# Kernel optimization log

Hardware: AMD Instinct MI355X
Metric: run time of the kernel (lower is better)

Reference implementation:

```python
import jax, jax.numpy as jnp
import numpy as np
import math

B, L, D_IN, H, N, NL, D_OUT = 16, 4096, 64, 256, 32, 4, 10
EPS = 1e-5


def setup_inputs() -> dict:
    key = jax.random.key(0)
    ks = jax.random.split(key, 16)
    inp = {}
    inp['x'] = jax.random.normal(ks[0], (B, L, D_IN), dtype=jnp.float32)
    inp['enc_w'] = jax.random.normal(ks[1], (H, D_IN), dtype=jnp.float32) / math.sqrt(D_IN)
    inp['enc_b'] = jax.random.normal(ks[2], (H,), dtype=jnp.float32) * 0.01
    # log_dt uniform in [log(1e-3), log(1e-1)] as in S4D init
    inp['log_dt'] = jax.random.uniform(ks[3], (NL, H), dtype=jnp.float32,
                                       minval=math.log(1e-3), maxval=math.log(1e-1))
    inp['log_A_real'] = jnp.full((NL, H, N), math.log(0.5), dtype=jnp.float32)
    inp['A_imag'] = jnp.broadcast_to(math.pi * jnp.arange(N, dtype=jnp.float32), (NL, H, N)).copy()
    inp['C_re'] = jax.random.normal(ks[4], (NL, H, N), dtype=jnp.float32)
    inp['C_im'] = jax.random.normal(ks[5], (NL, H, N), dtype=jnp.float32)
    inp['D'] = jax.random.normal(ks[6], (NL, H), dtype=jnp.float32)
    inp['out_w'] = jax.random.normal(ks[7], (NL, 2 * H, H), dtype=jnp.float32) / math.sqrt(H)
    inp['out_b'] = jax.random.normal(ks[8], (NL, 2 * H), dtype=jnp.float32) * 0.01
    inp['ln_w'] = jnp.ones((NL, H), dtype=jnp.float32)
    inp['ln_b'] = jnp.zeros((NL, H), dtype=jnp.float32)
    inp['dec_w'] = jax.random.normal(ks[9], (D_OUT, H), dtype=jnp.float32) / math.sqrt(H)
    inp['dec_b'] = jax.random.normal(ks[10], (D_OUT,), dtype=jnp.float32) * 0.01
    return inp


def _s4d_kernel(log_dt, log_A_real, A_imag, C_re, C_im, length):
    # log_dt: (H,), others: (H, N). Returns real conv kernel (H, length).
    dt = jnp.exp(log_dt)[:, None]                       # (H, 1)
    A = -jnp.exp(log_A_real) + 1j * A_imag              # (H, N), Re(A) < 0
    dtA = A * dt                                        # (H, N)
    C = (C_re + 1j * C_im) * (jnp.expm1(dtA)) / A       # ZOH-style scaling
    t = jnp.arange(length, dtype=jnp.float32)
    vand = jnp.exp(dtA[:, :, None] * t)                 # (H, N, L) Vandermonde
    K = 2.0 * jnp.real(jnp.einsum('hn,hnl->hl', C, vand))
    return K


def _fft_conv(u, k):
    # u: (B, H, L), k: (H, L) -> causal circular-padded conv, (B, H, L)
    length = u.shape[-1]
    k_f = jnp.fft.rfft(k, n=2 * length)                 # (H, L+1)
    u_f = jnp.fft.rfft(u, n=2 * length)                 # (B, H, L+1)
    return jnp.fft.irfft(u_f * k_f[None], n=2 * length)[..., :length]


def _layernorm_channels(x, w, b):
    # x: (B, H, L), normalize over channel dim H
    mu = jnp.mean(x, axis=1, keepdims=True)
    var = jnp.var(x, axis=1, keepdims=True)
    return (x - mu) * jax.lax.rsqrt(var + EPS) * w[None, :, None] + b[None, :, None]


def reference(x, enc_w, enc_b, log_dt, log_A_real, A_imag, C_re, C_im, D,
              out_w, out_b, ln_w, ln_b, dec_w, dec_b):
    # encoder: (B, L, d_input) -> (B, L, H), then transpose -> (B, H, L)
    h = jnp.einsum('bli,hi->blh', x, enc_w) + enc_b
    h = jnp.swapaxes(h, -1, -2)                         # (B, H, L)
    length = h.shape[-1]
    for i in range(NL):
        z = h
        K = _s4d_kernel(log_dt[i], log_A_real[i], A_imag[i], C_re[i], C_im[i], length)
        y = _fft_conv(z, K) + z * D[i][None, :, None]   # SSM conv + skip
        y = jax.nn.gelu(y)
        # position-wise 1x1 conv to 2H, then GLU over channel dim
        g = jnp.einsum('bhl,gh->bgl', y, out_w[i]) + out_b[i][None, :, None]
        g1, g2 = jnp.split(g, 2, axis=1)
        y = g1 * jax.nn.sigmoid(g2)
        h = y + h                                       # residual (dropout=0)
        h = _layernorm_channels(h, ln_w[i], ln_b[i])    # post-norm
    h = jnp.swapaxes(h, -1, -2)                         # (B, L, H)
    return jnp.einsum('blh,oh->blo', h, dec_w) + dec_b
```

## Files before the change

kernel.cpp:

```cpp
#include <hip/hip_runtime.h>
#include <hip/hip_fp16.h>

#define B_   16
#define L_   4096
#define DIN  64
#define H_   256
#define N_   32
#define NL_  4
#define DOUT 10
#define CH_  32
#define T_   128

typedef _Float16 half8 __attribute__((ext_vector_type(8)));
typedef float f32x4 __attribute__((ext_vector_type(4)));

__device__ __forceinline__ float gelu_f(float v) {
    float t3  = v * v * v;
    float arg = 0.7978845608028654f * fmaf(0.044715f, t3, v);
    float e   = __expf(2.f * arg);
    float th  = 1.f - 2.f / (e + 1.f);
    return 0.5f * v * (1.f + th);
}

__global__ __launch_bounds__(256) void gen_k(
    const float* __restrict__ log_dt, const float* __restrict__ log_A_real,
    const float* __restrict__ A_imag, const float* __restrict__ C_re, const float* __restrict__ C_im,
    const float* __restrict__ Dp,
    _Float16* __restrict__ Wv, _Float16* __restrict__ Vt, _Float16* __restrict__ G,
    float* __restrict__ wtr, float* __restrict__ wti)
{
    __shared__ float sxr[N_], sxi[N_], scr[N_], sci[N_], skd[T_];
    int ih = blockIdx.x;
    int t  = threadIdx.x;
    if (t < N_) {
        int n = t;
        float dt  = expf(log_dt[ih]);
        float Are = -expf(log_A_real[ih * N_ + n]);
        float Aim = A_imag[ih * N_ + n];
        float xr = dt * Are, xi = dt * Aim;
        float ex = expf(xr), cy = cosf(xi), sy = sinf(xi);
        float sh = sinf(0.5f * xi);
        float em_re = expm1f(xr) * cy - 2.f * sh * sh;
        float em_im = ex * sy;
        float inv = 1.f / (Are * Are + Aim * Aim);
        float qr = (em_re * Are + em_im * Aim) * inv;
        float qi = (em_im * Are - em_re * Aim) * inv;
        float crv = C_re[ih * N_ + n], civ = C_im[ih * N_ + n];
        sxr[n] = xr; sxi[n] = xi;
        scr[n] = 2.f * (crv * qr - civ * qi);
        sci[n] = 2.f * (crv * qi + civ * qr);
        float txr = 128.f * xr, txi = 128.f * xi;
        float exT = expf(txr);
        wtr[ih * N_ + n] = exT * cosf(txi);
        wti[ih * N_ + n] = exT * sinf(txi);
    }
    __syncthreads();
    if (t <= T_) {
        int d = t;
        float fd = (float)d;
        float kd = 0.f;
        for (int n = 0; n < N_; n++) {
            float ar = expf(fd * sxr[n]);
            float ang = fd * sxi[n];
            float wdr = ar * cosf(ang), wdi = ar * sinf(ang);
            if (d < T_) {
                kd = fmaf(scr[n], wdr, kd);
                kd = fmaf(-sci[n], wdi, kd);
                Wv[((size_t)ih * 64 + 2 * n) * T_ + (127 - d)]     = (_Float16)wdr;
                Wv[((size_t)ih * 64 + 2 * n + 1) * T_ + (127 - d)] = (_Float16)wdi;
            }
            if (d >= 1) {
                float vr = scr[n] * wdr - sci[n] * wdi;
                float vi = scr[n] * wdi + sci[n] * wdr;
                Vt[((size_t)ih * T_ + (d - 1)) * 64 + 2 * n]     = (_Float16)vr;
                Vt[((size_t)ih * T_ + (d - 1)) * 64 + 2 * n + 1] = (_Float16)(-vi);
            }
        }
        if (d < T_) skd[d] = kd;
    }
    __syncthreads();
    if (t < T_) {
        float v = skd[127 - t];
        if (t == 127) v += Dp[ih];
        G[(size_t)ih * 256 + t]       = (_Float16)v;
        G[(size_t)ih * 256 + 128 + t] = (_Float16)0.f;
    }
}

__global__ __launch_bounds__(256) void wconv_k(const float* __restrict__ w, _Float16* __restrict__ w16)
{
    int idx = blockIdx.x * 256 + threadIdx.x;
    w16[idx] = (_Float16)w[idx];
}

__global__ __launch_bounds__(256) void encoder_k(
    const float* __restrict__ x, const float* __restrict__ ew,
    const float* __restrict__ eb, _Float16* __restrict__ z16)
{
    __shared__ float xt[64][64];
    int blk = blockIdx.x;
    int b  = blk >> 6;
    int l0 = (blk & 63) << 6;
    int t  = threadIdx.x;
    {
        int r = t >> 2, cp = (t & 3) * 16;
        const float4* src = (const float4*)(x + ((size_t)(b * L_ + l0 + r)) * DIN + cp);
        float4* dst = (float4*)&xt[r][cp];
#pragma unroll
        for (int j = 0; j < 4; j++) dst[j] = src[j];
    }
    float wrg[64];
#pragma unroll
    for (int i = 0; i < 64; i += 4) {
        float4 wv = *(const float4*)(ew + t * 64 + i);
        wrg[i] = wv.x; wrg[i+1] = wv.y; wrg[i+2] = wv.z; wrg[i+3] = wv.w;
    }
    float bias = eb[t];
    __syncthreads();
    _Float16* outz = z16 + ((size_t)(b * H_ + t)) * L_ + l0;
    for (int l = 0; l < 64; l += 4) {
        _Float16 h4[4];
#pragma unroll
        for (int q = 0; q < 4; q++) {
            float a0 = 0.f, a1 = 0.f;
#pragma unroll
            for (int i = 0; i < 64; i += 2) {
                a0 = fmaf(xt[l+q][i],   wrg[i],   a0);
                a1 = fmaf(xt[l+q][i+1], wrg[i+1], a1);
            }
            h4[q] = (_Float16)(a0 + a1 + bias);
        }
        *(uint2*)(outz + l) = *(uint2*)h4;
    }
}

__global__ __launch_bounds__(256) void finals_k(
    const _Float16* __restrict__ z16, const _Float16* __restrict__ Wv,
    const float* __restrict__ wtr, const float* __restrict__ wti,
    _Float16* __restrict__ Sinit)
{
    __shared__ _Float16 zb[CH_][136];
    __shared__ float Fs[CH_][68];
    int h = blockIdx.x, b = blockIdx.y;
    int t = threadIdx.x;
    const uint4* src = (const uint4*)(z16 + ((size_t)(b * H_ + h)) * L_);
#pragma unroll
    for (int j = 0; j < 2; j++) {
        uint4 v = src[t * 2 + j];
        int e0 = (t * 2 + j) * 8;
        *(uint4*)&zb[e0 >> 7][e0 & 127] = v;
    }
    __syncthreads();
    int lane = t & 63, w = t >> 6;
    int l15 = lane & 15, quad = lane >> 4;
    f32x4 acc[2];
    acc[0] = (f32x4){0.f,0.f,0.f,0.f};
    acc[1] = (f32x4){0.f,0.f,0.f,0.f};
    const _Float16* wvb = Wv + ((size_t)h * 64 + w * 16 + l15) * T_;
#pragma unroll
    for (int ks = 0; ks < 4; ks++) {
        int kk = ks * 32 + quad * 8;
        half8 a  = *(const half8*)(wvb + kk);
        half8 b0 = *(const half8*)&zb[l15][kk];
        half8 b1 = *(const half8*)&zb[16 + l15][kk];
        acc[0] = __builtin_amdgcn_mfma_f32_16x16x32_f16(a, b0, acc[0], 0, 0, 0);
        acc[1] = __builtin_amdgcn_mfma_f32_16x16x32_f16(a, b1, acc[1], 0, 0, 0);
    }
#pragma unroll
    for (int nt = 0; nt < 2; nt++) {
        int c = nt * 16 + l15;
        *(f32x4*)&Fs[c][w * 16 + quad * 4] = acc[nt];
    }
    __syncthreads();
    if (t < N_) {
        int n = t;
        float wr = wtr[h * N_ + n], wi = wti[h * N_ + n];
        float cr = 0.f, ci = 0.f;
        _Float16* sb = Sinit + ((size_t)(b * H_ + h)) * (CH_ * 64) + 2 * n;
        for (int c = 0; c < CH_; c++) {
            float2 f2 = *(const float2*)&Fs[c][2 * n];
            union { unsigned u; _Float16 hf[2]; } p;
            p.hf[0] = (_Float16)cr; p.hf[1] = (_Float16)ci;
            *(unsigned*)(sb + (size_t)c * 64) = p.u;
            float nr = fmaf(wr, cr, f2.x);
            nr = fmaf(-wi, ci, nr);
            float ni = fmaf(wi, cr, f2.y);
            ni = fmaf(wr, ci, ni);
            cr = nr; ci = ni;
        }
    }
}

__global__ __launch_bounds__(256) void conv_k(
    const _Float16* __restrict__ z16, const _Float16* __restrict__ G,
    const _Float16* __restrict__ Vt, const _Float16* __restrict__ Sinit,
    _Float16* __restrict__ y16)
{
    __shared__ _Float16 zT[128][136];
    __shared__ _Float16 Ff[128][72];
    __shared__ _Float16 Gs[256];
    int h = blockIdx.x, rb = blockIdx.y;
    int t = threadIdx.x;
    int b0 = rb * 4;
#pragma unroll
    for (int q = 0; q < 8; q++) {
        int idx = q * 256 + t;
        int brow = idx >> 9;
        int e = (idx & 511) * 8;
        uint4 v = *(const uint4*)(z16 + ((size_t)((b0 + brow) * H_ + h)) * L_ + e);
        int c = e >> 7, jj = e & 127;
        *(uint4*)&zT[brow * 32 + c][jj] = v;
    }
#pragma unroll
    for (int q = 0; q < 4; q++) {
        int idx = q * 256 + t;
        int e0 = idx * 8;
        int brow = e0 >> 11;
        int off = e0 & 2047;
        uint4 v = *(const uint4*)(Sinit + ((size_t)((b0 + brow) * H_ + h)) * (CH_ * 64) + off);
        int r = brow * 32 + (off >> 6), k = off & 63;
        *(uint4*)&Ff[r][k] = v;
    }
    Gs[t] = G[(size_t)h * 256 + t];
    __syncthreads();
    int lane = t & 63, w = t >> 6;
    int l15 = lane & 15, quad = lane >> 4;
    f32x4 acc[2][8];
#pragma unroll
    for (int mt = 0; mt < 2; mt++)
#pragma unroll
        for (int nt = 0; nt < 8; nt++) acc[mt][nt] = (f32x4){0.f,0.f,0.f,0.f};
#pragma unroll
    for (int ks = 0; ks < 4; ks++) {
        int kk = ks * 32 + quad * 8;
        int base0 = 127 - (w * 32 + l15) + kk;
        int base1 = base0 - 16;
        half8 a0, a1;
#pragma unroll
        for (int j = 0; j < 8; j++) { a0[j] = Gs[base0 + j]; a1[j] = Gs[base1 + j]; }
#pragma unroll
        for (int nt = 0; nt < 8; nt++) {
            half8 bf = *(const half8*)&zT[nt * 16 + l15][kk];
            acc[0][nt] = __builtin_amdgcn_mfma_f32_16x16x32_f16(a0, bf, acc[0][nt], 0, 0, 0);
            acc[1][nt] = __builtin_amdgcn_mfma_f32_16x16x32_f16(a1, bf, acc[1][nt], 0, 0, 0);
        }
    }
    const _Float16* vb = Vt + (size_t)h * T_ * 64;
#pragma unroll
    for (int ks = 0; ks < 2; ks++) {
        int kk = ks * 32 + quad * 8;
        half8 a0 = *(const half8*)(vb + ((size_t)(w * 32 + l15)) * 64 + kk);
        half8 a1 = *(const half8*)(vb + ((size_t)(w * 32 + 16 + l15)) * 64 + kk);
#pragma unroll
        for (int nt = 0; nt < 8; nt++) {
            half8 bf = *(const half8*)&Ff[nt * 16 + l15][kk];
            acc[0][nt] = __builtin_amdgcn_mfma_f32_16x16x32_f16(a0, bf, acc[0][nt], 0, 0, 0);
            acc[1][nt] = __builtin_amdgcn_mfma_f32_16x16x32_f16(a1, bf, acc[1][nt], 0, 0, 0);
        }
    }
    __syncthreads();
#pragma unroll
    for (int mt = 0; mt < 2; mt++)
#pragma unroll
        for (int nt = 0; nt < 8; nt++) {
            int r = nt * 16 + l15;
            int tt0 = w * 32 + mt * 16 + quad * 4;
            _Float16 o[4];
#pragma unroll
            for (int rr = 0; rr < 4; rr++) o[rr] = (_Float16)gelu_f(acc[mt][nt][rr]);
            *(uint2*)&zT[r][tt0] = *(uint2*)o;
        }
    __syncthreads();
#pragma unroll
    for (int q = 0; q < 8; q++) {
        int idx = q * 256 + t;
        int brow = idx >> 9;
        int e = (idx & 511) * 8;
        int c = e >> 7, jj = e & 127;
        uint4 v = *(uint4*)&zT[brow * 32 + c][jj];
        *(uint4*)(y16 + ((size_t)((b0 + brow) * H_ + h)) * L_ + e) = v;
    }
}

__global__ __launch_bounds__(256, 2) void glu_k(
    const _Float16* __restrict__ W, const _Float16* __restrict__ y16,
    const float* __restrict__ outb, const float* __restrict__ lnw,
    const float* __restrict__ lnb, _Float16* __restrict__ z16)
{
    __shared__ float u_s[256 * 66];
    __shared__ float red[2][4][64];
    __shared__ float mus[64], rss[64];
    _Float16* yT = (_Float16*)u_s;
    int b  = blockIdx.y;
    int l0 = blockIdx.x << 6;
    int t  = threadIdx.x;
    int lane = t & 63, wid = t >> 6;
    int l15 = lane & 15, quad = lane >> 4;
    {
        const uint4* src = (const uint4*)(y16 + ((size_t)(b * H_ + t)) * L_ + l0);
        uint4 v[8];
#pragma unroll
        for (int j = 0; j < 8; j++) v[j] = src[j];
        const _Float16* hv = (const _Float16*)v;
#pragma unroll
        for (int j = 0; j < 64; j++) yT[j * 264 + t] = hv[j];
    }
    __syncthreads();
    f32x4 acc[8][4];
#pragma unroll
    for (int mt = 0; mt < 8; mt++)
#pragma unroll
        for (int nt = 0; nt < 4; nt++) acc[mt][nt] = (f32x4){0.f,0.f,0.f,0.f};
#pragma unroll
    for (int ks = 0; ks < 8; ks++) {
        int kk = ks * 32 + quad * 8;
        half8 bf[4];
#pragma unroll
        for (int nt = 0; nt < 4; nt++) bf[nt] = *(const half8*)&yT[(nt * 16 + l15) * 264 + kk];
#pragma unroll
        for (int mt = 0; mt < 8; mt++) {
            int row = (mt >> 2) * 256 + wid * 64 + (mt & 3) * 16 + l15;
            half8 a = *(const half8*)(W + (size_t)row * H_ + kk);
#pragma unroll
            for (int nt = 0; nt < 4; nt++)
                acc[mt][nt] = __builtin_amdgcn_mfma_f32_16x16x32_f16(a, bf[nt], acc[mt][nt], 0, 0, 0);
        }
    }
    __syncthreads();
#pragma unroll
    for (int mt = 0; mt < 4; mt++) {
        int chb = wid * 64 + mt * 16 + quad * 4;
        float4 ob1 = *(const float4*)(outb + chb);
        float4 ob2 = *(const float4*)(outb + 256 + chb);
        const float* o1 = (const float*)&ob1;
        const float* o2 = (const float*)&ob2;
#pragma unroll
        for (int nt = 0; nt < 4; nt++) {
            int l = nt * 16 + l15;
#pragma unroll
            for (int r = 0; r < 4; r++) {
                float g1 = acc[mt][nt][r] + o1[r];
                float g2 = acc[mt + 4][nt][r] + o2[r];
                float sg = 1.f / (1.f + __expf(-g2));
                u_s[(chb + r) * 66 + l] = g1 * sg;
            }
        }
    }
    __syncthreads();
    int lr = t & 63, grp = t >> 6;
    float s1 = 0.f, s2 = 0.f;
    for (int j = 0; j < 64; j++) {
        int ch = grp * 64 + j;
        float uu = u_s[ch * 66 + lr] + (float)z16[((size_t)(b * H_ + ch)) * L_ + l0 + lr];
        u_s[ch * 66 + lr] = uu;
        s1 += uu; s2 = fmaf(uu, uu, s2);
    }
    red[0][grp][lr] = s1; red[1][grp][lr] = s2;
    __syncthreads();
    if (t < 64) {
        float a = red[0][0][t] + red[0][1][t] + red[0][2][t] + red[0][3][t];
        float q = red[1][0][t] + red[1][1][t] + red[1][2][t] + red[1][3][t];
        float mu  = a * (1.f / 256.f);
        float var = q * (1.f / 256.f) - mu * mu;
        mus[t] = mu; rss[t] = rsqrtf(var + 1e-5f);
    }
    __syncthreads();
    int lg = (t & 15) * 4, ch0 = t >> 4;
    float mu4[4], rs4[4];
#pragma unroll
    for (int i = 0; i < 4; i++) { mu4[i] = mus[lg + i]; rs4[i] = rss[lg + i]; }
#pragma unroll
    for (int j = 0; j < 16; j++) {
        int ch = ch0 + 16 * j;
        float wv = lnw[ch], bv = lnb[ch];
        _Float16 o4[4];
#pragma unroll
        for (int i = 0; i < 4; i++) {
            float vv = (u_s[ch * 66 + lg + i] - mu4[i]) * rs4[i] * wv + bv;
            o4[i] = (_Float16)vv;
        }
        *(uint2*)(z16 + ((size_t)(b * H_ + ch)) * L_ + l0 + lg) = *(uint2*)o4;
    }
}

__global__ __launch_bounds__(256) void decoder_k(
    const _Float16* __restrict__ z16, const float* __restrict__ dw,
    const float* __restrict__ db, float* __restrict__ out)
{
    __shared__ float ht[256][65];
    __shared__ float wt[DOUT * H_];
    int blk = blockIdx.x;
    int b  = blk >> 6;
    int l0 = (blk & 63) << 6;
    int t  = threadIdx.x;
    {
        const uint4* src = (const uint4*)(z16 + ((size_t)(b * H_ + t)) * L_ + l0);
        uint4 v[8];
#pragma unroll
        for (int j = 0; j < 8; j++) v[j] = src[j];
        const _Float16* hv = (const _Float16*)v;
#pragma unroll
        for (int j = 0; j < 64; j++) ht[t][j] = (float)hv[j];
    }
    for (int idx = t; idx < DOUT * H_; idx += 256) wt[idx] = dw[idx];
    __syncthreads();
    int l = t & 63, og = t >> 6;
    for (int o = og; o < DOUT; o += 4) {
        float a0 = 0.f, a1 = 0.f;
#pragma unroll 8
        for (int k = 0; k < H_; k += 2) {
            a0 = fmaf(ht[k][l],     wt[o * H_ + k],     a0);
            a1 = fmaf(ht[k + 1][l], wt[o * H_ + k + 1], a1);
        }
        out[((size_t)(b * L_ + l0 + l)) * DOUT + o] = a0 + a1 + db[o];
    }
}

extern "C" void kernel_launch(void* const* d_in, const int* in_sizes, int n_in,
                              void* d_out, int out_size, void* d_ws, size_t ws_size,
                              hipStream_t stream)
{
    (void)in_sizes; (void)n_in; (void)out_size; (void)ws_size;
    const float* x          = (const float*)d_in[0];
    const float* enc_w      = (const float*)d_in[1];
    const float* enc_b      = (const float*)d_in[2];
    const float* log_dt     = (const float*)d_in[3];
    const float* log_A_real = (const float*)d_in[4];
    const float* A_imag     = (const float*)d_in[5];
    const float* C_re       = (const float*)d_in[6];
    const float* C_im       = (const float*)d_in[7];
    const float* Dp         = (const float*)d_in[8];
    const float* out_w      = (const float*)d_in[9];
    const float* out_b      = (const float*)d_in[10];
    const float* ln_w       = (const float*)d_in[11];
    const float* ln_b       = (const float*)d_in[12];
    const float* dec_w      = (const float*)d_in[13];
    const float* dec_b      = (const float*)d_in[14];
    float* outp = (float*)d_out;

    char* ws = (char*)d_ws;
    _Float16* z16 = (_Float16*)ws;   ws += (size_t)B_ * H_ * L_ * 2;
    _Float16* y16 = (_Float16*)ws;   ws += (size_t)B_ * H_ * L_ * 2;
    _Float16* Sinit = (_Float16*)ws; ws += (size_t)B_ * H_ * CH_ * 64 * 2;
    _Float16* Wv = (_Float16*)ws;    ws += (size_t)NL_ * H_ * 64 * T_ * 2;
    _Float16* Vt = (_Float16*)ws;    ws += (size_t)NL_ * H_ * T_ * 64 * 2;
    _Float16* G  = (_Float16*)ws;    ws += (size_t)NL_ * H_ * 256 * 2;
    size_t tb = (size_t)NL_ * H_ * N_;
    float* wtr = (float*)ws; ws += tb * 4;
    float* wti = (float*)ws; ws += tb * 4;
    _Float16* W16 = (_Float16*)ws; ws += (size_t)NL_ * 2 * H_ * H_ * 2;

    gen_k<<<NL_ * H_, 256, 0, stream>>>(log_dt, log_A_real, A_imag, C_re, C_im, Dp,
                                        Wv, Vt, G, wtr, wti);
    wconv_k<<<(NL_ * 2 * H_ * H_) / 256, 256, 0, stream>>>(out_w, W16);
    encoder_k<<<B_ * 64, 256, 0, stream>>>(x, enc_w, enc_b, z16);
    for (int i = 0; i < NL_; i++) {
        size_t th = (size_t)i * H_;
        finals_k<<<dim3(H_, B_), 256, 0, stream>>>(z16, Wv + th * 64 * T_,
                                                   wtr + th * N_, wti + th * N_, Sinit);
        conv_k<<<dim3(H_, B_ / 4), 256, 0, stream>>>(z16, G + th * 256, Vt + th * T_ * 64,
                                                     Sinit, y16);
        glu_k<<<dim3(L_ / 64, B_), 256, 0, stream>>>(W16 + (size_t)i * 2 * H_ * H_, y16,
                                                     out_b + i * 2 * H_, ln_w + th, ln_b + th, z16);
    }
    decoder_k<<<B_ * 64, 256, 0, stream>>>(z16, dec_w, dec_b, outp);
}
```

Measured before the change: 611.1 us.

## Move encoder and decoder projections onto fp16 MFMA matrix instructions

Rewrites the encoder to stage x and enc_w as fp16 in shared memory and compute the 64-to-256 projection with 16x16x32 MFMA tiles over 128-position blocks, writing the result back through a shared transpose. The decoder likewise transposes z into shared memory and uses MFMA against a zero-padded fp16 copy of dec_w, which a new one-block prep kernel builds. The aim is to replace scalar FMA loops in these two kernels with matrix-core throughput. In exchange, x and the weights are rounded to fp16 before accumulation, and an extra kernel launch is added.

```diff
diff --git a/kernel.cpp b/kernel.cpp
--- a/kernel.cpp
+++ b/kernel.cpp
@@ -12,6 +12,7 @@
 #define T_   128
 
 typedef _Float16 half8 __attribute__((ext_vector_type(8)));
+typedef _Float16 half4 __attribute__((ext_vector_type(4)));
 typedef float f32x4 __attribute__((ext_vector_type(4)));
 
 __device__ __forceinline__ float gelu_f(float v) {
@@ -93,44 +94,87 @@
     w16[idx] = (_Float16)w[idx];
 }
 
+__global__ __launch_bounds__(256) void dprep_k(const float* __restrict__ dw, _Float16* __restrict__ dwp)
+{
+    int t = threadIdx.x;
+#pragma unroll
+    for (int j = 0; j < 16; j++) {
+        int idx = j * 256 + t;
+        dwp[idx] = (idx < DOUT * H_) ? (_Float16)dw[idx] : (_Float16)0.f;
+    }
+}
+
 __global__ __launch_bounds__(256) void encoder_k(
     const float* __restrict__ x, const float* __restrict__ ew,
     const float* __restrict__ eb, _Float16* __restrict__ z16)
 {
-    __shared__ float xt[64][64];
-    int blk = blockIdx.x;
-    int b  = blk >> 6;
-    int l0 = (blk & 63) << 6;
+    __shared__ _Float16 smem[35840];
+    _Float16* xs  = smem;
+    _Float16* ews = smem + 128 * 72;
+    _Float16* ot  = smem;
+    int b  = blockIdx.y;
+    int l0 = blockIdx.x << 7;
     int t  = threadIdx.x;
-    {
-        int r = t >> 2, cp = (t & 3) * 16;
-        const float4* src = (const float4*)(x + ((size_t)(b * L_ + l0 + r)) * DIN + cp);
-        float4* dst = (float4*)&xt[r][cp];
-#pragma unroll
-        for (int j = 0; j < 4; j++) dst[j] = src[j];
-    }
-    float wrg[64];
-#pragma unroll
-    for (int i = 0; i < 64; i += 4) {
-        float4 wv = *(const float4*)(ew + t * 64 + i);
-        wrg[i] = wv.x; wrg[i+1] = wv.y; wrg[i+2] = wv.z; wrg[i+3] = wv.w;
-    }
-    float bias = eb[t];
-    __syncthreads();
-    _Float16* outz = z16 + ((size_t)(b * H_ + t)) * L_ + l0;
-    for (int l = 0; l < 64; l += 4) {
-        _Float16 h4[4];
-#pragma unroll
-        for (int q = 0; q < 4; q++) {
-            float a0 = 0.f, a1 = 0.f;
-#pragma unroll
-            for (int i = 0; i < 64; i += 2) {
-                a0 = fmaf(xt[l+q][i],   wrg[i],   a0);
-                a1 = fmaf(xt[l+q][i+1], wrg[i+1], a1);
-            }
-            h4[q] = (_Float16)(a0 + a1 + bias);
-        }
-        *(uint2*)(outz + l) = *(uint2*)h4;
+#pragma unroll
+    for (int j = 0; j < 8; j++) {
+        int idx = j * 256 + t;
+        int l = idx >> 4, i4 = (idx & 15) * 4;
+        float4 v = *(const float4*)(x + ((size_t)(b * L_ + l0 + l)) * DIN + i4);
+        _Float16 c[4] = {(_Float16)v.x, (_Float16)v.y, (_Float16)v.z, (_Float16)v.w};
+        *(uint2*)&xs[l * 72 + i4] = *(uint2*)c;
+    }
+#pragma unroll
+    for (int j = 0; j < 16; j++) {
+        int idx = j * 256 + t;
+        int h = idx >> 4, i4 = (idx & 15) * 4;
+        float4 v = *(const float4*)(ew + h * 64 + i4);
+        _Float16 c[4] = {(_Float16)v.x, (_Float16)v.y, (_Float16)v.z, (_Float16)v.w};
+        *(uint2*)&ews[h * 72 + i4] = *(uint2*)c;
+    }
+    __syncthreads();
+    int lane = t & 63, wid = t >> 6;
+    int l15 = lane & 15, quad = lane >> 4;
+    f32x4 acc[4][8];
+#pragma unroll
+    for (int mt = 0; mt < 4; mt++)
+#pragma unroll
+        for (int nt = 0; nt < 8; nt++) acc[mt][nt] = (f32x4){0.f,0.f,0.f,0.f};
+#pragma unroll
+    for (int ks = 0; ks < 2; ks++) {
+        int kk = ks * 32 + quad * 8;
+        half8 a[4], bb[8];
+#pragma unroll
+        for (int mt = 0; mt < 4; mt++)
+            a[mt] = *(const half8*)&ews[(wid * 64 + mt * 16 + l15) * 72 + kk];
+#pragma unroll
+        for (int nt = 0; nt < 8; nt++)
+            bb[nt] = *(const half8*)&xs[(nt * 16 + l15) * 72 + kk];
+#pragma unroll
+        for (int mt = 0; mt < 4; mt++)
+#pragma unroll
+            for (int nt = 0; nt < 8; nt++)
+                acc[mt][nt] = __builtin_amdgcn_mfma_f32_16x16x32_f16(a[mt], bb[nt], acc[mt][nt], 0, 0, 0);
+    }
+    __syncthreads();
+#pragma unroll
+    for (int mt = 0; mt < 4; mt++) {
+        int hb = wid * 64 + mt * 16 + quad * 4;
+        float b0 = eb[hb], b1 = eb[hb + 1], b2 = eb[hb + 2], b3 = eb[hb + 3];
+#pragma unroll
+        for (int nt = 0; nt < 8; nt++) {
+            int l = nt * 16 + l15;
+            ot[(hb + 0) * 136 + l] = (_Float16)(acc[mt][nt][0] + b0);
+            ot[(hb + 1) * 136 + l] = (_Float16)(acc[mt][nt][1] + b1);
+            ot[(hb + 2) * 136 + l] = (_Float16)(acc[mt][nt][2] + b2);
+            ot[(hb + 3) * 136 + l] = (_Float16)(acc[mt][nt][3] + b3);
+        }
+    }
+    __syncthreads();
+#pragma unroll
+    for (int p = 0; p < 16; p++) {
+        int row = p * 16 + (t >> 4), seg = t & 15;
+        uint4 v = *(uint4*)&ot[row * 136 + seg * 8];
+        *(uint4*)(z16 + ((size_t)(b * H_ + row)) * L_ + l0 + seg * 8) = v;
     }
 }
 
@@ -384,35 +428,53 @@
 }
 
 __global__ __launch_bounds__(256) void decoder_k(
-    const _Float16* __restrict__ z16, const float* __restrict__ dw,
+    const _Float16* __restrict__ z16, const _Float16* __restrict__ dwp,
     const float* __restrict__ db, float* __restrict__ out)
 {
-    __shared__ float ht[256][65];
-    __shared__ float wt[DOUT * H_];
-    int blk = blockIdx.x;
-    int b  = blk >> 6;
-    int l0 = (blk & 63) << 6;
+    __shared__ _Float16 zT[128][268];
+    int b  = blockIdx.y;
+    int l0 = blockIdx.x << 7;
     int t  = threadIdx.x;
-    {
-        const uint4* src = (const uint4*)(z16 + ((size_t)(b * H_ + t)) * L_ + l0);
-        uint4 v[8];
-#pragma unroll
-        for (int j = 0; j < 8; j++) v[j] = src[j];
-        const _Float16* hv = (const _Float16*)v;
-#pragma unroll
-        for (int j = 0; j < 64; j++) ht[t][j] = (float)hv[j];
-    }
-    for (int idx = t; idx < DOUT * H_; idx += 256) wt[idx] = dw[idx];
-    __syncthreads();
-    int l = t & 63, og = t >> 6;
-    for (int o = og; o < DOUT; o += 4) {
-        float a0 = 0.f, a1 = 0.f;
 #pragma unroll 8
-        for (int k = 0; k < H_; k += 2) {
-            a0 = fmaf(ht[k][l],     wt[o * H_ + k],     a0);
-            a1 = fmaf(ht[k + 1][l], wt[o * H_ + k + 1], a1);
-        }
-        out[((size_t)(b * L_ + l0 + l)) * DOUT + o] = a0 + a1 + db[o];
+    for (int j = 0; j < 64; j++) {
+        int idx = j * 256 + t;
+        int h = idx >> 6, lp = idx & 63;
+        unsigned v = *(const unsigned*)(z16 + ((size_t)(b * H_ + h)) * L_ + l0 + lp * 2);
+        union { unsigned u; _Float16 f[2]; } c; c.u = v;
+        zT[lp * 2][h]     = c.f[0];
+        zT[lp * 2 + 1][h] = c.f[1];
+    }
+    __syncthreads();
+    int lane = t & 63, wid = t >> 6;
+    int l15 = lane & 15, quad = lane >> 4;
+    f32x4 acc[2];
+    acc[0] = (f32x4){0.f,0.f,0.f,0.f};
+    acc[1] = (f32x4){0.f,0.f,0.f,0.f};
+#pragma unroll
+    for (int ks = 0; ks < 8; ks++) {
+        int kk = ks * 32 + quad * 8;
+        half8 a = *(const half8*)(dwp + l15 * 256 + kk);
+#pragma unroll
+        for (int nt = 0; nt < 2; nt++) {
+            int l = (wid * 2 + nt) * 16 + l15;
+            half4 lo = *(const half4*)&zT[l][kk];
+            half4 hi = *(const half4*)&zT[l][kk + 4];
+            half8 bf;
+#pragma unroll
+            for (int j = 0; j < 4; j++) { bf[j] = lo[j]; bf[j + 4] = hi[j]; }
+            acc[nt] = __builtin_amdgcn_mfma_f32_16x16x32_f16(a, bf, acc[nt], 0, 0, 0);
+        }
+    }
+    int o0 = quad * 4;
+#pragma unroll
+    for (int nt = 0; nt < 2; nt++) {
+        int l = (wid * 2 + nt) * 16 + l15;
+        float* op = out + ((size_t)(b * L_ + l0 + l)) * DOUT;
+#pragma unroll
+        for (int r = 0; r < 4; r++) {
+            int o = o0 + r;
+            if (o < DOUT) op[o] = acc[nt][r] + db[o];
+        }
     }
 }
 
@@ -449,11 +511,13 @@
     float* wtr = (float*)ws; ws += tb * 4;
     float* wti = (float*)ws; ws += tb * 4;
     _Float16* W16 = (_Float16*)ws; ws += (size_t)NL_ * 2 * H_ * H_ * 2;
+    _Float16* dwp = (_Float16*)ws; ws += (size_t)16 * H_ * 2;
 
     gen_k<<<NL_ * H_, 256, 0, stream>>>(log_dt, log_A_real, A_imag, C_re, C_im, Dp,
                                         Wv, Vt, G, wtr, wti);
     wconv_k<<<(NL_ * 2 * H_ * H_) / 256, 256, 0, stream>>>(out_w, W16);
-    encoder_k<<<B_ * 64, 256, 0, stream>>>(x, enc_w, enc_b, z16);
+    dprep_k<<<1, 256, 0, stream>>>(dec_w, dwp);
+    encoder_k<<<dim3(L_ / 128, B_), 256, 0, stream>>>(x, enc_w, enc_b, z16);
     for (int i = 0; i < NL_; i++) {
         size_t th = (size_t)i * H_;
         finals_k<<<dim3(H_, B_), 256, 0, stream>>>(z16, Wv + th * 64 * T_,
@@ -463,5 +527,5 @@
         glu_k<<<dim3(L_ / 64, B_), 256, 0, stream>>>(W16 + (size_t)i * 2 * H_ * H_, y16,
                                                      out_b + i * 2 * H_, ln_w + th, ln_b + th, z16);
     }
-    decoder_k<<<B_ * 64, 256, 0, stream>>>(z16, dec_w, dec_b, outp);
-}
+    decoder_k<<<dim3(L_ / 128, B_), 256, 0, stream>>>(z16, dwp, dec_b, outp);
+}
```

After: 550.6 us. 1.11x faster.
